# Kernel tuning notes

Hardware: AMD Instinct MI355X
Metric: run time of the kernel (lower is better)

Reference implementation:

```python
import jax, jax.numpy as jnp
import numpy as np

N_NODES = 50000
N_EDGES = 600000
D_IN = 128
D_HID = 1024
D_OUT = 128


def setup_inputs() -> dict:
    key = jax.random.key(0)
    ks = jax.random.split(key, 8)
    feat = jax.random.normal(ks[0], (N_NODES, D_IN), dtype=jnp.float32)
    edge_feat = jax.random.normal(ks[1], (N_EDGES, D_IN), dtype=jnp.float32)
    src = jax.random.randint(ks[2], (N_EDGES,), 0, N_NODES, dtype=jnp.int32)
    dst = jax.random.randint(ks[3], (N_EDGES,), 0, N_NODES, dtype=jnp.int32)
    W1 = jax.random.normal(ks[4], (D_IN, D_HID), dtype=jnp.float32) * (1.0 / np.sqrt(D_IN))
    b1 = jnp.zeros((D_HID,), dtype=jnp.float32)
    W2 = jax.random.normal(ks[5], (D_HID, D_OUT), dtype=jnp.float32) * (1.0 / np.sqrt(D_HID))
    b2 = jnp.zeros((D_OUT,), dtype=jnp.float32)
    return {"feat": feat, "edge_feat": edge_feat, "src": src, "dst": dst,
            "W1": W1, "b1": b1, "W2": W2, "b2": b2}


def reference(feat, edge_feat, src, dst, W1, b1, W2, b2):
    # DGL u_add_e: message m_e = h_src(e) + e_feat(e)   [E, D_IN]
    messages = feat[src] + edge_feat
    # reduce sum over incoming edges at each destination node -> [N, D_IN]
    h = jax.ops.segment_sum(messages, dst, num_segments=N_NODES)
    # 2-layer MLP
    h = jax.nn.relu(h @ W1 + b1)
    return h @ W2 + b2
```

## Files before the change

### kernel.cpp

```cpp
#include <hip/hip_runtime.h>
#include <hip/hip_bf16.h>

#define N_NODES 50000
#define N_EDGES 600000
#define D_IN    128
#define D_HID   1024
#define D_OUT   128

#define WS_PAIRS  0
#define WS_OFF    4800000
#define WS_CURSOR 5000016
#define WS_DEG    5200016
#define WS_BSUM   5400016
#define WS_W1T    5401040
#define WS_W2T    5663184

typedef short bf16x8 __attribute__((ext_vector_type(8)));
typedef short s16x4  __attribute__((ext_vector_type(4)));
typedef float f32x4  __attribute__((ext_vector_type(4)));
typedef int   i32x2  __attribute__((ext_vector_type(2)));

__global__ __launch_bounds__(256) void hist_kernel(
    const int* __restrict__ dst, int* __restrict__ deg)
{
    int e = blockIdx.x * blockDim.x + threadIdx.x;
    if (e < N_EDGES) atomicAdd(&deg[dst[e]], 1);
}

__global__ __launch_bounds__(256) void scan1_kernel(
    const int* __restrict__ deg, int* __restrict__ bsum)
{
    __shared__ int red[256];
    int t = threadIdx.x;
    int idx = blockIdx.x * 256 + t;
    red[t] = (idx < N_NODES) ? deg[idx] : 0;
    __syncthreads();
    for (int s = 128; s > 0; s >>= 1) {
        if (t < s) red[t] += red[t + s];
        __syncthreads();
    }
    if (t == 0) bsum[blockIdx.x] = red[0];
}

#define SCAN_NB 196
__global__ __launch_bounds__(256) void scan2_kernel(
    int* __restrict__ bsum, int* __restrict__ off)
{
    __shared__ int sh[256];
    int t = threadIdx.x;
    int v = (t < SCAN_NB) ? bsum[t] : 0;
    sh[t] = v;
    __syncthreads();
    for (int ofs = 1; ofs < 256; ofs <<= 1) {
        int u = (t >= ofs) ? sh[t - ofs] : 0;
        __syncthreads();
        sh[t] += u;
        __syncthreads();
    }
    if (t < SCAN_NB) bsum[t] = sh[t] - v;
    if (t == 255) off[N_NODES] = sh[255];
}

__global__ __launch_bounds__(256) void scan3_kernel(
    const int* __restrict__ deg, const int* __restrict__ bsum,
    int* __restrict__ off, int* __restrict__ cursor)
{
    __shared__ int sh[256];
    int t = threadIdx.x;
    int idx = blockIdx.x * 256 + t;
    int v = (idx < N_NODES) ? deg[idx] : 0;
    sh[t] = v;
    __syncthreads();
    for (int ofs = 1; ofs < 256; ofs <<= 1) {
        int u = (t >= ofs) ? sh[t - ofs] : 0;
        __syncthreads();
        sh[t] += u;
        __syncthreads();
    }
    if (idx < N_NODES) {
        int ex = bsum[blockIdx.x] + sh[t] - v;
        off[idx] = ex;
        cursor[idx] = ex;
    }
}

__global__ __launch_bounds__(256) void fill_kernel(
    const int* __restrict__ dst, const int* __restrict__ src,
    int* __restrict__ cursor, int* __restrict__ pairs)
{
    int e = blockIdx.x * blockDim.x + threadIdx.x;
    if (e < N_EDGES) {
        int s = src[e];
        int pos = atomicAdd(&cursor[dst[e]], 1);
        i32x2 v; v.x = e; v.y = s;
        *(i32x2*)(pairs + 2 * (size_t)pos) = v;
    }
}

__global__ __launch_bounds__(256) void transpose_cvt2_kernel(
    const float* __restrict__ W1, __hip_bfloat16* __restrict__ w1t,
    const float* __restrict__ W2, __hip_bfloat16* __restrict__ w2t)
{
    __shared__ float tile[32][33];
    int b = blockIdx.x;
    const float* in;
    __hip_bfloat16* outp;
    int rows, cols, c0, r0;
    if (b < 128) {
        in = W1; outp = w1t; rows = D_IN; cols = D_HID;
        c0 = (b & 31) * 32; r0 = (b >> 5) * 32;
    } else {
        int bb = b - 128;
        in = W2; outp = w2t; rows = D_HID; cols = D_OUT;
        c0 = (bb & 3) * 32; r0 = (bb >> 2) * 32;
    }
    int tx = threadIdx.x & 31, ty = threadIdx.x >> 5;
    #pragma unroll
    for (int i = 0; i < 32; i += 8)
        tile[ty + i][tx] = in[(size_t)(r0 + ty + i) * cols + (c0 + tx)];
    __syncthreads();
    #pragma unroll
    for (int i = 0; i < 32; i += 8)
        outp[(size_t)(c0 + ty + i) * rows + (r0 + tx)] =
            __float2bfloat16(tile[tx][ty + i]);
}

#define HS_STRIDE 136
#define QS_STRIDE 72

__global__ __launch_bounds__(256) void fused_gnn_kernel(
    const float* __restrict__ feat,
    const float* __restrict__ edge_feat,
    const int*   __restrict__ pairs,
    const int*   __restrict__ off,
    const __hip_bfloat16* __restrict__ w1t,
    const float* __restrict__ b1,
    const __hip_bfloat16* __restrict__ w2t,
    const float* __restrict__ b2,
    float* __restrict__ out)
{
    __shared__ __align__(16) short h_s[64 * HS_STRIDE];
    __shared__ __align__(16) short q_s[2][64 * QS_STRIDE];

    const int t    = threadIdx.x;
    const int wv   = t >> 6;
    const int lane = t & 63;
    const int half = lane >> 4;
    const int lid  = lane & 15;
    const int nb   = blockIdx.x * 64;

    const short* w1s = (const short*)w1t;
    const short* w2s = (const short*)w2t;

    const int eh = lane >> 5;
    const int ln = lane & 31;

    int my_off = 0;
    {
        int oidx = nb + wv * 16 + lane;
        if (lane <= 16) {
            int c = oidx > N_NODES ? N_NODES : oidx;
            my_off = off[c];
        }
    }

    for (int j = 0; j < 16; ++j) {
        const int r = wv * 16 + j;
        int base = __builtin_amdgcn_readfirstlane(__shfl(my_off, j));
        int end  = __builtin_amdgcn_readfirstlane(__shfl(my_off, j + 1));

        f32x4 a0 = f32x4{0.f,0.f,0.f,0.f}, a1 = a0, a2 = a0, a3 = a0;
        int i = base;
        for (; i + 8 <= end; i += 8) {
            i32x2 p0 = *(const i32x2*)(pairs + 2 * (size_t)(i + 0 + eh));
            i32x2 p1 = *(const i32x2*)(pairs + 2 * (size_t)(i + 2 + eh));
            i32x2 p2 = *(const i32x2*)(pairs + 2 * (size_t)(i + 4 + eh));
            i32x2 p3 = *(const i32x2*)(pairs + 2 * (size_t)(i + 6 + eh));
            f32x4 e0 = *(const f32x4*)(edge_feat + (size_t)p0.x * D_IN + ln * 4);
            f32x4 g0 = *(const f32x4*)(feat      + (size_t)p0.y * D_IN + ln * 4);
            f32x4 e1 = *(const f32x4*)(edge_feat + (size_t)p1.x * D_IN + ln * 4);
            f32x4 g1 = *(const f32x4*)(feat      + (size_t)p1.y * D_IN + ln * 4);
            f32x4 e2 = *(const f32x4*)(edge_feat + (size_t)p2.x * D_IN + ln * 4);
            f32x4 g2 = *(const f32x4*)(feat      + (size_t)p2.y * D_IN + ln * 4);
            f32x4 e3 = *(const f32x4*)(edge_feat + (size_t)p3.x * D_IN + ln * 4);
            f32x4 g3 = *(const f32x4*)(feat      + (size_t)p3.y * D_IN + ln * 4);
            a0 += e0 + g0;
            a1 += e1 + g1;
            a2 += e2 + g2;
            a3 += e3 + g3;
        }
        for (; i + 4 <= end; i += 4) {
            i32x2 p0 = *(const i32x2*)(pairs + 2 * (size_t)(i + 0 + eh));
            i32x2 p1 = *(const i32x2*)(pairs + 2 * (size_t)(i + 2 + eh));
            f32x4 e0 = *(const f32x4*)(edge_feat + (size_t)p0.x * D_IN + ln * 4);
            f32x4 g0 = *(const f32x4*)(feat      + (size_t)p0.y * D_IN + ln * 4);
            f32x4 e1 = *(const f32x4*)(edge_feat + (size_t)p1.x * D_IN + ln * 4);
            f32x4 g1 = *(const f32x4*)(feat      + (size_t)p1.y * D_IN + ln * 4);
            a0 += e0 + g0;
            a1 += e1 + g1;
        }
        for (; i < end; i += 2) {
            if (i + eh < end) {
                i32x2 p = *(const i32x2*)(pairs + 2 * (size_t)(i + eh));
                f32x4 e = *(const f32x4*)(edge_feat + (size_t)p.x * D_IN + ln * 4);
                f32x4 g = *(const f32x4*)(feat      + (size_t)p.y * D_IN + ln * 4);
                a0 += e + g;
            }
        }
        f32x4 s = (a0 + a1) + (a2 + a3);
        s[0] += __shfl_xor(s[0], 32);
        s[1] += __shfl_xor(s[1], 32);
        s[2] += __shfl_xor(s[2], 32);
        s[3] += __shfl_xor(s[3], 32);
        if (eh == 0) {
            s16x4 hv;
            __hip_bfloat16 b0 = __float2bfloat16(s[0]); hv[0] = *(short*)&b0;
            __hip_bfloat16 c1 = __float2bfloat16(s[1]); hv[1] = *(short*)&c1;
            __hip_bfloat16 c2 = __float2bfloat16(s[2]); hv[2] = *(short*)&c2;
            __hip_bfloat16 c3 = __float2bfloat16(s[3]); hv[3] = *(short*)&c3;
            *(s16x4*)&h_s[r * HS_STRIDE + ln * 4] = hv;
        }
    }
    __syncthreads();

    bf16x8 afrag[4][4];
    #pragma unroll
    for (int mt = 0; mt < 4; ++mt)
        #pragma unroll
        for (int ks = 0; ks < 4; ++ks)
            afrag[mt][ks] = *(const bf16x8*)&h_s[(mt * 16 + lid) * HS_STRIDE + ks * 32 + half * 8];

    f32x4 acc[4][2];
    #pragma unroll
    for (int mt = 0; mt < 4; ++mt) {
        acc[mt][0] = f32x4{0.f, 0.f, 0.f, 0.f};
        acc[mt][1] = f32x4{0.f, 0.f, 0.f, 0.f};
    }

    const int ncol1 = wv * 16 + lid;

    int pb = 0;
    for (int jb = 0; jb < D_HID; jb += 64, pb ^= 1) {
        float bias = b1[jb + ncol1];
        bf16x8 bfrag[4];
        #pragma unroll
        for (int ks = 0; ks < 4; ++ks)
            bfrag[ks] = *(const bf16x8*)&w1s[(size_t)(jb + ncol1) * 128 + ks * 32 + half * 8];

        f32x4 c1[4];
        #pragma unroll
        for (int mt = 0; mt < 4; ++mt) {
            f32x4 c = f32x4{bias, bias, bias, bias};
            #pragma unroll
            for (int ks = 0; ks < 4; ++ks)
                c = __builtin_amdgcn_mfma_f32_16x16x32_bf16(afrag[mt][ks], bfrag[ks], c, 0, 0, 0);
            c1[mt] = c;
        }

        #pragma unroll
        for (int mt = 0; mt < 4; ++mt) {
            #pragma unroll
            for (int r = 0; r < 4; ++r) {
                float v = fmaxf(c1[mt][r], 0.f);
                __hip_bfloat16 bv = __float2bfloat16(v);
                q_s[pb][(mt * 16 + half * 4 + r) * QS_STRIDE + wv * 16 + lid] = *(short*)&bv;
            }
        }
        __syncthreads();

        bf16x8 a2f[4][2];
        #pragma unroll
        for (int mt = 0; mt < 4; ++mt)
            #pragma unroll
            for (int ks = 0; ks < 2; ++ks)
                a2f[mt][ks] = *(const bf16x8*)&q_s[pb][(mt * 16 + lid) * QS_STRIDE + ks * 32 + half * 8];

        #pragma unroll
        for (int nt = 0; nt < 2; ++nt) {
            #pragma unroll
            for (int ks = 0; ks < 2; ++ks) {
                bf16x8 b2f = *(const bf16x8*)&w2s[(size_t)(wv * 32 + nt * 16 + lid) * 1024 + jb + ks * 32 + half * 8];
                #pragma unroll
                for (int mt = 0; mt < 4; ++mt)
                    acc[mt][nt] = __builtin_amdgcn_mfma_f32_16x16x32_bf16(a2f[mt][ks], b2f, acc[mt][nt], 0, 0, 0);
            }
        }
    }

    #pragma unroll
    for (int nt = 0; nt < 2; ++nt) {
        int col = wv * 32 + nt * 16 + lid;
        float bv = b2[col];
        #pragma unroll
        for (int mt = 0; mt < 4; ++mt) {
            #pragma unroll
            for (int r = 0; r < 4; ++r) {
                int row = nb + mt * 16 + half * 4 + r;
                if (row < N_NODES)
                    out[(size_t)row * D_OUT + col] = acc[mt][nt][r] + bv;
            }
        }
    }
}

extern "C" void kernel_launch(void* const* d_in, const int* in_sizes, int n_in,
                              void* d_out, int out_size, void* d_ws, size_t ws_size,
                              hipStream_t stream) {
    const float* feat      = (const float*)d_in[0];
    const float* edge_feat = (const float*)d_in[1];
    const int*   src       = (const int*)d_in[2];
    const int*   dst       = (const int*)d_in[3];
    const float* W1        = (const float*)d_in[4];
    const float* b1        = (const float*)d_in[5];
    const float* W2        = (const float*)d_in[6];
    const float* b2        = (const float*)d_in[7];
    float* out = (float*)d_out;

    char* ws = (char*)d_ws;
    int*   pairs  = (int*)(ws + WS_PAIRS);
    int*   off    = (int*)(ws + WS_OFF);
    int*   cursor = (int*)(ws + WS_CURSOR);
    int*   deg    = (int*)(ws + WS_DEG);
    int*   bsum   = (int*)(ws + WS_BSUM);
    __hip_bfloat16* w1t = (__hip_bfloat16*)(ws + WS_W1T);
    __hip_bfloat16* w2t = (__hip_bfloat16*)(ws + WS_W2T);

    hipMemsetAsync(deg, 0, (size_t)N_NODES * sizeof(int), stream);

    hist_kernel<<<(N_EDGES + 255) / 256, 256, 0, stream>>>(dst, deg);
    scan1_kernel<<<SCAN_NB, 256, 0, stream>>>(deg, bsum);
    scan2_kernel<<<1, 256, 0, stream>>>(bsum, off);
    scan3_kernel<<<SCAN_NB, 256, 0, stream>>>(deg, bsum, off, cursor);
    fill_kernel<<<(N_EDGES + 255) / 256, 256, 0, stream>>>(dst, src, cursor, pairs);

    transpose_cvt2_kernel<<<256, 256, 0, stream>>>(W1, w1t, W2, w2t);

    fused_gnn_kernel<<<(N_NODES + 63) / 64, 256, 0, stream>>>(
        feat, edge_feat, pairs, off, w1t, b1, w2t, b2, out);
}
```

Measured before the change: 636.1 us.

## Gather edges as a flat stream across 16 rows per wave with float2 lanes

The per-row edge loop, which split each row's edges across two half-waves and reduced them with a shuffle, is replaced by one flat loop over all edges of the wave's 16 destination rows. Each lane now loads a float2, so all 64 lanes cover the 128 features of a single edge, and the row is flushed to shared memory when the edge index crosses a row boundary. Row offsets are staged in shared memory. This avoids per-row tail loops and under-filled 8-edge batches on low-degree rows, keeping more loads in flight. The cost is narrower 8-byte loads and data-dependent flush branches inside the unrolled loop.

```diff
diff --git a/kernel.cpp b/kernel.cpp
--- a/kernel.cpp
+++ b/kernel.cpp
@@ -16,7 +16,6 @@
 #define WS_W2T    5663184
 
 typedef short bf16x8 __attribute__((ext_vector_type(8)));
-typedef short s16x4  __attribute__((ext_vector_type(4)));
 typedef float f32x4  __attribute__((ext_vector_type(4)));
 typedef int   i32x2  __attribute__((ext_vector_type(2)));
 
@@ -141,6 +140,7 @@
 {
     __shared__ __align__(16) short h_s[64 * HS_STRIDE];
     __shared__ __align__(16) short q_s[2][64 * QS_STRIDE];
+    __shared__ int off_s[65];
 
     const int t    = threadIdx.x;
     const int wv   = t >> 6;
@@ -152,74 +152,86 @@
     const short* w1s = (const short*)w1t;
     const short* w2s = (const short*)w2t;
 
-    const int eh = lane >> 5;
-    const int ln = lane & 31;
-
-    int my_off = 0;
+    if (t < 65) {
+        int oidx = nb + t;
+        off_s[t] = off[oidx > N_NODES ? N_NODES : oidx];
+    }
+    __syncthreads();
+
     {
-        int oidx = nb + wv * 16 + lane;
-        if (lane <= 16) {
-            int c = oidx > N_NODES ? N_NODES : oidx;
-            my_off = off[c];
-        }
-    }
-
-    for (int j = 0; j < 16; ++j) {
-        const int r = wv * 16 + j;
-        int base = __builtin_amdgcn_readfirstlane(__shfl(my_off, j));
-        int end  = __builtin_amdgcn_readfirstlane(__shfl(my_off, j + 1));
-
-        f32x4 a0 = f32x4{0.f,0.f,0.f,0.f}, a1 = a0, a2 = a0, a3 = a0;
-        int i = base;
+        const int r0  = wv * 16;
+        int cur = r0;
+        int nxt = off_s[r0 + 1];
+        const int i0  = off_s[r0];
+        const int end = off_s[r0 + 16];
+        float2 acc = make_float2(0.f, 0.f);
+
+        #define FLUSH_ROW() do {                                            \
+            __hip_bfloat162 hv_;                                            \
+            hv_.x = __float2bfloat16(acc.x);                                \
+            hv_.y = __float2bfloat16(acc.y);                                \
+            *(__hip_bfloat162*)&h_s[cur * HS_STRIDE + lane * 2] = hv_;      \
+            acc.x = 0.f; acc.y = 0.f;                                       \
+            ++cur; nxt = off_s[cur + 1];                                    \
+        } while (0)
+
+        #define EDGE_ACC(K, EV, GV) do {                                    \
+            while (i + (K) >= nxt) FLUSH_ROW();                             \
+            acc.x += EV.x + GV.x;                                           \
+            acc.y += EV.y + GV.y;                                           \
+        } while (0)
+
+        int i = i0;
         for (; i + 8 <= end; i += 8) {
-            i32x2 p0 = *(const i32x2*)(pairs + 2 * (size_t)(i + 0 + eh));
-            i32x2 p1 = *(const i32x2*)(pairs + 2 * (size_t)(i + 2 + eh));
-            i32x2 p2 = *(const i32x2*)(pairs + 2 * (size_t)(i + 4 + eh));
-            i32x2 p3 = *(const i32x2*)(pairs + 2 * (size_t)(i + 6 + eh));
-            f32x4 e0 = *(const f32x4*)(edge_feat + (size_t)p0.x * D_IN + ln * 4);
-            f32x4 g0 = *(const f32x4*)(feat      + (size_t)p0.y * D_IN + ln * 4);
-            f32x4 e1 = *(const f32x4*)(edge_feat + (size_t)p1.x * D_IN + ln * 4);
-            f32x4 g1 = *(const f32x4*)(feat      + (size_t)p1.y * D_IN + ln * 4);
-            f32x4 e2 = *(const f32x4*)(edge_feat + (size_t)p2.x * D_IN + ln * 4);
-            f32x4 g2 = *(const f32x4*)(feat      + (size_t)p2.y * D_IN + ln * 4);
-            f32x4 e3 = *(const f32x4*)(edge_feat + (size_t)p3.x * D_IN + ln * 4);
-            f32x4 g3 = *(const f32x4*)(feat      + (size_t)p3.y * D_IN + ln * 4);
-            a0 += e0 + g0;
-            a1 += e1 + g1;
-            a2 += e2 + g2;
-            a3 += e3 + g3;
-        }
-        for (; i + 4 <= end; i += 4) {
-            i32x2 p0 = *(const i32x2*)(pairs + 2 * (size_t)(i + 0 + eh));
-            i32x2 p1 = *(const i32x2*)(pairs + 2 * (size_t)(i + 2 + eh));
-            f32x4 e0 = *(const f32x4*)(edge_feat + (size_t)p0.x * D_IN + ln * 4);
-            f32x4 g0 = *(const f32x4*)(feat      + (size_t)p0.y * D_IN + ln * 4);
-            f32x4 e1 = *(const f32x4*)(edge_feat + (size_t)p1.x * D_IN + ln * 4);
-            f32x4 g1 = *(const f32x4*)(feat      + (size_t)p1.y * D_IN + ln * 4);
-            a0 += e0 + g0;
-            a1 += e1 + g1;
-        }
-        for (; i < end; i += 2) {
-            if (i + eh < end) {
-                i32x2 p = *(const i32x2*)(pairs + 2 * (size_t)(i + eh));
-                f32x4 e = *(const f32x4*)(edge_feat + (size_t)p.x * D_IN + ln * 4);
-                f32x4 g = *(const f32x4*)(feat      + (size_t)p.y * D_IN + ln * 4);
-                a0 += e + g;
-            }
-        }
-        f32x4 s = (a0 + a1) + (a2 + a3);
-        s[0] += __shfl_xor(s[0], 32);
-        s[1] += __shfl_xor(s[1], 32);
-        s[2] += __shfl_xor(s[2], 32);
-        s[3] += __shfl_xor(s[3], 32);
-        if (eh == 0) {
-            s16x4 hv;
-            __hip_bfloat16 b0 = __float2bfloat16(s[0]); hv[0] = *(short*)&b0;
-            __hip_bfloat16 c1 = __float2bfloat16(s[1]); hv[1] = *(short*)&c1;
-            __hip_bfloat16 c2 = __float2bfloat16(s[2]); hv[2] = *(short*)&c2;
-            __hip_bfloat16 c3 = __float2bfloat16(s[3]); hv[3] = *(short*)&c3;
-            *(s16x4*)&h_s[r * HS_STRIDE + ln * 4] = hv;
-        }
+            i32x2 p0 = *(const i32x2*)(pairs + 2 * (size_t)(i + 0));
+            i32x2 p1 = *(const i32x2*)(pairs + 2 * (size_t)(i + 1));
+            i32x2 p2 = *(const i32x2*)(pairs + 2 * (size_t)(i + 2));
+            i32x2 p3 = *(const i32x2*)(pairs + 2 * (size_t)(i + 3));
+            i32x2 p4 = *(const i32x2*)(pairs + 2 * (size_t)(i + 4));
+            i32x2 p5 = *(const i32x2*)(pairs + 2 * (size_t)(i + 5));
+            i32x2 p6 = *(const i32x2*)(pairs + 2 * (size_t)(i + 6));
+            i32x2 p7 = *(const i32x2*)(pairs + 2 * (size_t)(i + 7));
+            float2 e0 = ((const float2*)(edge_feat + (size_t)p0.x * D_IN))[lane];
+            float2 g0 = ((const float2*)(feat      + (size_t)p0.y * D_IN))[lane];
+            float2 e1 = ((const float2*)(edge_feat + (size_t)p1.x * D_IN))[lane];
+            float2 g1 = ((const float2*)(feat      + (size_t)p1.y * D_IN))[lane];
+            float2 e2 = ((const float2*)(edge_feat + (size_t)p2.x * D_IN))[lane];
+            float2 g2 = ((const float2*)(feat      + (size_t)p2.y * D_IN))[lane];
+            float2 e3 = ((const float2*)(edge_feat + (size_t)p3.x * D_IN))[lane];
+            float2 g3 = ((const float2*)(feat      + (size_t)p3.y * D_IN))[lane];
+            float2 e4 = ((const float2*)(edge_feat + (size_t)p4.x * D_IN))[lane];
+            float2 g4 = ((const float2*)(feat      + (size_t)p4.y * D_IN))[lane];
+            float2 e5 = ((const float2*)(edge_feat + (size_t)p5.x * D_IN))[lane];
+            float2 g5 = ((const float2*)(feat      + (size_t)p5.y * D_IN))[lane];
+            float2 e6 = ((const float2*)(edge_feat + (size_t)p6.x * D_IN))[lane];
+            float2 g6 = ((const float2*)(feat      + (size_t)p6.y * D_IN))[lane];
+            float2 e7 = ((const float2*)(edge_feat + (size_t)p7.x * D_IN))[lane];
+            float2 g7 = ((const float2*)(feat      + (size_t)p7.y * D_IN))[lane];
+            EDGE_ACC(0, e0, g0);
+            EDGE_ACC(1, e1, g1);
+            EDGE_ACC(2, e2, g2);
+            EDGE_ACC(3, e3, g3);
+            EDGE_ACC(4, e4, g4);
+            EDGE_ACC(5, e5, g5);
+            EDGE_ACC(6, e6, g6);
+            EDGE_ACC(7, e7, g7);
+        }
+        for (; i < end; ++i) {
+            i32x2 p = *(const i32x2*)(pairs + 2 * (size_t)i);
+            float2 e = ((const float2*)(edge_feat + (size_t)p.x * D_IN))[lane];
+            float2 g = ((const float2*)(feat      + (size_t)p.y * D_IN))[lane];
+            EDGE_ACC(0, e, g);
+        }
+        while (cur < r0 + 16) {
+            __hip_bfloat162 hv_;
+            hv_.x = __float2bfloat16(acc.x);
+            hv_.y = __float2bfloat16(acc.y);
+            *(__hip_bfloat162*)&h_s[cur * HS_STRIDE + lane * 2] = hv_;
+            acc.x = 0.f; acc.y = 0.f;
+            ++cur;
+        }
+        #undef EDGE_ACC
+        #undef FLUSH_ROW
     }
     __syncthreads();
 
```

Result: no change. 637.8 us (+0.3%).
